# Performance work log

Measured on AMD Instinct MI355X. Metric: run time of the kernel, lower is better.

The kernel has to match this reference:

```python
import jax, jax.numpy as jnp
import numpy as np

B, T, D, H = 32, 2048, 1024, 128


def setup_inputs() -> dict:
    key = jax.random.key(0)
    ks = jax.random.split(key, 7)
    s = 1.0 / np.sqrt(D)
    return {
        "x": jax.random.normal(ks[0], (B, T, D), dtype=jnp.float32),
        "Wk": jax.random.normal(ks[1], (D, H), dtype=jnp.float32) * s,
        "bk": jax.random.normal(ks[2], (H,), dtype=jnp.float32) * 0.01,
        "Wq": jax.random.normal(ks[3], (D, H), dtype=jnp.float32) * s,
        "bq": jax.random.normal(ks[4], (H,), dtype=jnp.float32) * 0.01,
        "Wv": jax.random.normal(ks[5], (D, H), dtype=jnp.float32) * s,
        "bv": jax.random.normal(ks[6], (H,), dtype=jnp.float32) * 0.01,
    }


def reference(x, Wk, bk, Wq, bq, Wv, bv):
    # Single causal attention head. NOTE faithful quirk: scores = K @ Q^T.
    k = x @ Wk + bk  # [B,T,H]
    q = x @ Wq + bq  # [B,T,H]
    v = x @ Wv + bv  # [B,T,H]
    scale = k.shape[-1] ** -0.5
    wei = jnp.einsum("bth,bsh->bts", k, q) * scale  # [B,T,T], K on the left
    t = x.shape[1]
    causal = jnp.tril(jnp.ones((t, t), dtype=bool))
    wei = jnp.where(causal, wei, -jnp.inf)
    wei = jax.nn.softmax(wei, axis=-1)
    # dropout is eval-mode identity (deterministic reference)
    out = jnp.einsum("bts,bsh->bth", wei, v)  # [B,T,H]
    return out
```

## Files before the change

kernel.cpp:

```cpp
#include <hip/hip_runtime.h>
#include <hip/hip_bf16.h>
#include <stdint.h>

typedef __bf16 bf16;
typedef __bf16 bf16x8 __attribute__((ext_vector_type(8)));
typedef __bf16 bf16x4 __attribute__((ext_vector_type(4)));
typedef float f32x4 __attribute__((ext_vector_type(4)));
typedef float f32x8 __attribute__((ext_vector_type(8)));

#define BB 32
#define TT 2048
#define DD 1024
#define HH 128
#define SCALE 0.08838834764831845f
#define LOG2E 1.4426950408889634f
#define KS (SCALE * LOG2E)

__device__ __forceinline__ void gl_lds16(const bf16* g, bf16* l) {
  __builtin_amdgcn_global_load_lds((__attribute__((address_space(1))) const void*)g,
                                   (__attribute__((address_space(3))) void*)l,
                                   16, 0, 0);
}
__device__ __forceinline__ void gl_lds16f_nt(const float* g, float* l) {
  __builtin_amdgcn_global_load_lds((__attribute__((address_space(1))) const void*)g,
                                   (__attribute__((address_space(3))) void*)l,
                                   16, 0, 2);
}

__global__ __launch_bounds__(256) void prep_w(const float* __restrict__ Wk,
                                              const float* __restrict__ Wq,
                                              const float* __restrict__ Wv,
                                              const float* __restrict__ bk,
                                              const float* __restrict__ bq,
                                              const float* __restrict__ bv,
                                              bf16* __restrict__ Wt,
                                              float* __restrict__ bcat) {
  int tid = blockIdx.x * 256 + threadIdx.x;
  if (tid < 384) {
    int mat = tid >> 7, h = tid & 127;
    float bb = (mat == 0) ? bk[h] : (mat == 1) ? bq[h] : bv[h];
    bcat[tid] = (mat == 0) ? bb * KS : bb;
  }
  int mat = tid >> 14;
  int r = tid & 16383;
  int h = r & 127;
  int d0 = (r >> 7) << 3;
  const float* W = (mat == 0) ? Wk : (mat == 1) ? Wq : Wv;
  const float ks = (mat == 0) ? KS : 1.0f;
  bf16x8 v;
#pragma unroll
  for (int i = 0; i < 8; ++i) v[i] = (bf16)(W[(size_t)(d0 + i) * HH + h] * ks);
  *(bf16x8*)(Wt + ((size_t)mat * HH + h) * DD + d0) = v;
}

__global__ __launch_bounds__(256, 2) void qkv_proj(
    const float* __restrict__ x, const bf16* __restrict__ Wt,
    const float* __restrict__ bcat,
    bf16* __restrict__ kb, bf16* __restrict__ qb, bf16* __restrict__ Vt) {
  const int bid = blockIdx.x;
  const int tid = threadIdx.x;
  const int lane = tid & 63;
  const int w = tid >> 6;
  const int l15 = lane & 15, l4 = lane >> 4;
  const size_t row0 = (size_t)bid * 64;
  const int colbase = w * 96;

  __shared__ __attribute__((aligned(16))) float As[2][64][32];
  __shared__ __attribute__((aligned(16))) bf16  Ws[2][384][32];

  f32x4 acc[4][6];
#pragma unroll
  for (int m = 0; m < 4; ++m)
#pragma unroll
    for (int n = 0; n < 6; ++n) acc[m][n] = f32x4{0.f, 0.f, 0.f, 0.f};

  auto stage = [&](int buf, int k0) {
#pragma unroll
    for (int i = 0; i < 2; ++i) {
      int base = i * 256 + w * 64;
      int L = base + lane;
      int r = L >> 3, c = L & 7;
      const float* src = x + (row0 + r) * DD + k0 + ((c ^ (r & 7)) << 2);
      gl_lds16f_nt(src, &As[buf][0][0] + (size_t)base * 4);
    }
#pragma unroll
    for (int i = 0; i < 6; ++i) {
      int base = i * 256 + w * 64;
      int L = base + lane;
      int col = L >> 2, j = L & 3;
      const bf16* src = Wt + (size_t)col * DD + k0 + ((j ^ ((col >> 1) & 3)) << 3);
      gl_lds16(src, &Ws[buf][0][0] + (size_t)base * 8);
    }
  };

  stage(0, 0);
  __syncthreads();

  for (int step = 0; step < 32; ++step) {
    const int cur = step & 1;
    if (step + 1 < 32) stage(cur ^ 1, (step + 1) * 32);

    bf16x8 af[4];
#pragma unroll
    for (int m = 0; m < 4; ++m) {
      int r = m * 16 + l15;
      int c0 = (2 * l4) ^ (r & 7), c1 = (2 * l4 + 1) ^ (r & 7);
      f32x4 lo = *(const f32x4*)&As[cur][r][c0 * 4];
      f32x4 hi = *(const f32x4*)&As[cur][r][c1 * 4];
#pragma unroll
      for (int i = 0; i < 4; ++i) { af[m][i] = (bf16)lo[i]; af[m][4 + i] = (bf16)hi[i]; }
    }
    bf16x8 bfr[6];
#pragma unroll
    for (int n = 0; n < 6; ++n) {
      int col = colbase + n * 16 + l15;
      bfr[n] = *(const bf16x8*)&Ws[cur][col][(l4 ^ ((col >> 1) & 3)) * 8];
    }
#pragma unroll
    for (int m = 0; m < 4; ++m)
#pragma unroll
      for (int n = 0; n < 6; ++n)
        acc[m][n] = __builtin_amdgcn_mfma_f32_16x16x32_bf16(af[m], bfr[n],
                                                            acc[m][n], 0, 0, 0);
    __syncthreads();
  }

  float bvv[6];
#pragma unroll
  for (int n = 0; n < 6; ++n) bvv[n] = bcat[colbase + n * 16 + l15];

  const int bidx = bid >> 5;
  const int tloc0 = (bid & 31) * 64;
#pragma unroll
  for (int m = 0; m < 4; ++m)
#pragma unroll
    for (int n = 0; n < 6; ++n) {
      int col = colbase + n * 16 + l15;
      int mat = col >> 7;
      int hcol = col & 127;
      if (mat == 2) {
        bf16x4 v4;
#pragma unroll
        for (int e = 0; e < 4; ++e) v4[e] = (bf16)(acc[m][n][e] + bvv[n]);
        int t = tloc0 + m * 16 + l4 * 4;
        *(bf16x4*)(Vt + ((size_t)bidx * HH + hcol) * TT + t) = v4;
      } else {
        bf16* dst = (mat == 0) ? kb : qb;
#pragma unroll
        for (int e = 0; e < 4; ++e) {
          size_t rowg = row0 + m * 16 + l4 * 4 + e;
          dst[rowg * HH + hcol] = (bf16)(acc[m][n][e] + bvv[n]);
        }
      }
    }
}

__global__ __launch_bounds__(256, 3) void attn(const bf16* __restrict__ kb,
                                               const bf16* __restrict__ qb,
                                               const bf16* __restrict__ Vt,
                                               float* __restrict__ out) {
  const int bid = blockIdx.x;
  const int b = bid & 31;
  const int p = bid >> 5;
  const int tid = threadIdx.x;
  const int lane = tid & 63;
  const int w = tid >> 6;
  const int l15 = lane & 15, l4 = lane >> 4;

  __shared__ __attribute__((aligned(16))) bf16 Es[64 * 128];
  __shared__ __attribute__((aligned(16))) bf16 Vs[128 * 64];
  __shared__ __attribute__((aligned(16))) bf16 Ps[4][16 * 72];

  for (int job = 0; job < 2; ++job) {
    const int tile = job ? p : (31 - p);
    const int t0 = tile * 64;

    bf16x8 af[4];
    {
      const bf16* kp = kb + ((size_t)b * TT + t0 + w * 16 + l15) * HH + l4 * 8;
#pragma unroll
      for (int kc = 0; kc < 4; ++kc) af[kc] = *(const bf16x8*)(kp + kc * 32);
    }

    f32x4 o[8];
#pragma unroll
    for (int j = 0; j < 8; ++j) o[j] = f32x4{0.f, 0.f, 0.f, 0.f};
    float mrow[4], lrow[4];
#pragma unroll
    for (int e = 0; e < 4; ++e) { mrow[e] = -1e30f; lrow[e] = 0.f; }

    const int nst = tile + 1;
    for (int jt = 0; jt < nst; ++jt) {
      const int s0 = jt * 64;
      {
        const bf16* Eg = qb + ((size_t)b * TT + s0) * HH;
#pragma unroll
        for (int it = 0; it < 4; ++it) {
          int L = w * 256 + it * 64 + lane;
          int er = L >> 4, ec = L & 15;
          int ecs = ec ^ (er & 7);
          gl_lds16(Eg + er * HH + ecs * 8, Es + (size_t)(w * 256 + it * 64) * 8);
        }
        const bf16* Vg = Vt + (size_t)b * HH * TT + s0;
#pragma unroll
        for (int it = 0; it < 4; ++it) {
          int L = w * 256 + it * 64 + lane;
          int vr = L >> 3, vc = L & 7;
          int vcs = vc ^ (vr & 7);
          gl_lds16(Vg + (size_t)vr * TT + vcs * 8, Vs + (size_t)(w * 256 + it * 64) * 8);
        }
      }
      __syncthreads();

      f32x4 s[4];
#pragma unroll
      for (int j = 0; j < 4; ++j) s[j] = f32x4{0.f, 0.f, 0.f, 0.f};
#pragma unroll
      for (int kc = 0; kc < 4; ++kc) {
        bf16x8 ef[4];
#pragma unroll
        for (int fn = 0; fn < 4; ++fn) {
          int er = fn * 16 + l15;
          int c = kc * 4 + l4;
          int cs = c ^ (er & 7);
          ef[fn] = *(const bf16x8*)&Es[er * 128 + cs * 8];
        }
#pragma unroll
        for (int fn = 0; fn < 4; ++fn)
          s[fn] = __builtin_amdgcn_mfma_f32_16x16x32_bf16(af[kc], ef[fn],
                                                          s[fn], 0, 0, 0);
      }

      if (s0 + 63 > t0 + w * 16) {
#pragma unroll
        for (int fn = 0; fn < 4; ++fn)
#pragma unroll
          for (int e = 0; e < 4; ++e) {
            int tg = t0 + w * 16 + l4 * 4 + e;
            int sg = s0 + fn * 16 + l15;
            if (sg > tg) s[fn][e] = -1e30f;
          }
      }

      float mx[4];
#pragma unroll
      for (int e = 0; e < 4; ++e) {
        float m = fmaxf(fmaxf(s[0][e], s[1][e]), fmaxf(s[2][e], s[3][e]));
#pragma unroll
        for (int d = 1; d < 16; d <<= 1) m = fmaxf(m, __shfl_xor(m, d));
        mx[e] = m;
      }
      float g = fmaxf(fmaxf(mx[0] - mrow[0], mx[1] - mrow[1]),
                      fmaxf(mx[2] - mrow[2], mx[3] - mrow[3]));
      if (!__all(g <= 8.0f)) {
#pragma unroll
        for (int e = 0; e < 4; ++e) {
          float mn = fmaxf(mrow[e], mx[e]);
          float rsc = exp2f(mrow[e] - mn);
          lrow[e] *= rsc;
#pragma unroll
          for (int fh = 0; fh < 8; ++fh) o[fh][e] *= rsc;
          mrow[e] = mn;
        }
      }
#pragma unroll
      for (int e = 0; e < 4; ++e) {
        float ps = 0.f;
#pragma unroll
        for (int fn = 0; fn < 4; ++fn) {
          float pv = exp2f(s[fn][e] - mrow[e]);
          s[fn][e] = pv;
          ps += pv;
        }
#pragma unroll
        for (int d = 1; d < 16; d <<= 1) ps += __shfl_xor(ps, d);
        lrow[e] += ps;
      }

#pragma unroll
      for (int fn = 0; fn < 4; ++fn)
#pragma unroll
        for (int e = 0; e < 4; ++e)
          Ps[w][(l4 * 4 + e) * 72 + fn * 16 + l15] = (bf16)s[fn][e];

#pragma unroll
      for (int kc = 0; kc < 2; ++kc) {
        bf16x8 pf = *(const bf16x8*)&Ps[w][l15 * 72 + kc * 32 + l4 * 8];
#pragma unroll
        for (int fh = 0; fh < 8; ++fh) {
          int vr = fh * 16 + l15;
          int c = kc * 4 + l4;
          int cs = c ^ (vr & 7);
          bf16x8 vf = *(const bf16x8*)&Vs[vr * 64 + cs * 8];
          o[fh] = __builtin_amdgcn_mfma_f32_16x16x32_bf16(pf, vf, o[fh], 0, 0, 0);
        }
      }
      __syncthreads();
    }

#pragma unroll
    for (int e = 0; e < 4; ++e) {
      float rl = 1.0f / lrow[e];
      int tg = t0 + w * 16 + l4 * 4 + e;
#pragma unroll
      for (int fh = 0; fh < 8; ++fh)
        out[((size_t)b * TT + tg) * HH + fh * 16 + l15] = o[fh][e] * rl;
    }
  }
}

extern "C" void kernel_launch(void* const* d_in, const int* in_sizes, int n_in,
                              void* d_out, int out_size, void* d_ws, size_t ws_size,
                              hipStream_t stream) {
  (void)in_sizes; (void)n_in; (void)out_size; (void)ws_size;
  const float* x  = (const float*)d_in[0];
  const float* Wk = (const float*)d_in[1];
  const float* bk = (const float*)d_in[2];
  const float* Wq = (const float*)d_in[3];
  const float* bq = (const float*)d_in[4];
  const float* Wv = (const float*)d_in[5];
  const float* bv = (const float*)d_in[6];
  float* out = (float*)d_out;

  const size_t NTH = (size_t)BB * TT * HH;
  bf16* kb = (bf16*)d_ws;
  bf16* qb = kb + NTH;
  bf16* Vt = qb + NTH;
  bf16* Wt = Vt + NTH;
  float* bcat = (float*)(Wt + (size_t)3 * HH * DD);

  prep_w<<<192, 256, 0, stream>>>(Wk, Wq, Wv, bk, bq, bv, Wt, bcat);
  qkv_proj<<<1024, 256, 0, stream>>>(x, Wt, bcat, kb, qb, Vt);
  attn<<<512, 256, 0, stream>>>(kb, qb, Vt, out);
}
```

Before: 211.4 us.

## Enlarge QKV projection tile to 256 rows with 8 waves and bf16 x staging

The QKV projection now uses 512-thread blocks, each computing 256 rows by 384 columns, so every block of W staged into LDS is reused across four times as many rows. The x tile is loaded into registers, converted to bf16 once and written to a padded bf16 LDS buffer, replacing the direct fp32 global-to-LDS load and the per-wave conversions. This reduces repeated W loads and LDS footprint per row. In exchange the grid drops to 256 blocks (about one per CU), there are twice as many accumulators per wave, which raises register pressure, and x loads go through registers, which may expose their latency.

```diff
diff --git a/kernel.cpp b/kernel.cpp
--- a/kernel.cpp
+++ b/kernel.cpp
@@ -20,11 +20,6 @@
   __builtin_amdgcn_global_load_lds((__attribute__((address_space(1))) const void*)g,
                                    (__attribute__((address_space(3))) void*)l,
                                    16, 0, 0);
-}
-__device__ __forceinline__ void gl_lds16f_nt(const float* g, float* l) {
-  __builtin_amdgcn_global_load_lds((__attribute__((address_space(1))) const void*)g,
-                                   (__attribute__((address_space(3))) void*)l,
-                                   16, 0, 2);
 }
 
 __global__ __launch_bounds__(256) void prep_w(const float* __restrict__ Wk,
@@ -53,7 +48,7 @@
   *(bf16x8*)(Wt + ((size_t)mat * HH + h) * DD + d0) = v;
 }
 
-__global__ __launch_bounds__(256, 2) void qkv_proj(
+__global__ __launch_bounds__(512, 2) void qkv_proj(
     const float* __restrict__ x, const bf16* __restrict__ Wt,
     const float* __restrict__ bcat,
     bf16* __restrict__ kb, bf16* __restrict__ qb, bf16* __restrict__ Vt) {
@@ -61,67 +56,79 @@
   const int tid = threadIdx.x;
   const int lane = tid & 63;
   const int w = tid >> 6;
+  const int wr = w >> 2, wc = w & 3;
   const int l15 = lane & 15, l4 = lane >> 4;
-  const size_t row0 = (size_t)bid * 64;
-  const int colbase = w * 96;
-
-  __shared__ __attribute__((aligned(16))) float As[2][64][32];
-  __shared__ __attribute__((aligned(16))) bf16  Ws[2][384][32];
-
-  f32x4 acc[4][6];
-#pragma unroll
-  for (int m = 0; m < 4; ++m)
+  const size_t row0 = (size_t)bid * 256;
+  const int colbase = wc * 96;
+  const int rowbase = wr * 128;
+
+  __shared__ __attribute__((aligned(16))) bf16 As[2][256][40];
+  __shared__ __attribute__((aligned(16))) bf16 Ws[2][384 * 32];
+
+  const int sxr = tid >> 1, sxh = (tid & 1) * 16;
+
+  f32x4 acc[8][6];
+#pragma unroll
+  for (int m = 0; m < 8; ++m)
 #pragma unroll
     for (int n = 0; n < 6; ++n) acc[m][n] = f32x4{0.f, 0.f, 0.f, 0.f};
 
-  auto stage = [&](int buf, int k0) {
-#pragma unroll
-    for (int i = 0; i < 2; ++i) {
-      int base = i * 256 + w * 64;
-      int L = base + lane;
-      int r = L >> 3, c = L & 7;
-      const float* src = x + (row0 + r) * DD + k0 + ((c ^ (r & 7)) << 2);
-      gl_lds16f_nt(src, &As[buf][0][0] + (size_t)base * 4);
-    }
-#pragma unroll
-    for (int i = 0; i < 6; ++i) {
-      int base = i * 256 + w * 64;
+  auto stage_w = [&](int buf, int k0) {
+#pragma unroll
+    for (int i = 0; i < 3; ++i) {
+      int base = i * 512 + (w << 6);
       int L = base + lane;
       int col = L >> 2, j = L & 3;
       const bf16* src = Wt + (size_t)col * DD + k0 + ((j ^ ((col >> 1) & 3)) << 3);
-      gl_lds16(src, &Ws[buf][0][0] + (size_t)base * 8);
+      gl_lds16(src, &Ws[buf][0] + (size_t)base * 8);
     }
   };
-
-  stage(0, 0);
+  auto write_x = [&](int buf, f32x8 a0, f32x8 a1) {
+    bf16x8 t0, t1;
+#pragma unroll
+    for (int i = 0; i < 8; ++i) { t0[i] = (bf16)a0[i]; t1[i] = (bf16)a1[i]; }
+    *(bf16x8*)&As[buf][sxr][sxh] = t0;
+    *(bf16x8*)&As[buf][sxr][sxh + 8] = t1;
+  };
+
+  {
+    const float* src = x + (row0 + sxr) * DD + sxh;
+    f32x8 a0 = *(const f32x8*)src;
+    f32x8 a1 = *(const f32x8*)(src + 8);
+    stage_w(0, 0);
+    write_x(0, a0, a1);
+  }
   __syncthreads();
 
   for (int step = 0; step < 32; ++step) {
     const int cur = step & 1;
-    if (step + 1 < 32) stage(cur ^ 1, (step + 1) * 32);
-
-    bf16x8 af[4];
-#pragma unroll
-    for (int m = 0; m < 4; ++m) {
-      int r = m * 16 + l15;
-      int c0 = (2 * l4) ^ (r & 7), c1 = (2 * l4 + 1) ^ (r & 7);
-      f32x4 lo = *(const f32x4*)&As[cur][r][c0 * 4];
-      f32x4 hi = *(const f32x4*)&As[cur][r][c1 * 4];
-#pragma unroll
-      for (int i = 0; i < 4; ++i) { af[m][i] = (bf16)lo[i]; af[m][4 + i] = (bf16)hi[i]; }
-    }
+    const int k0 = step * 32;
+
+    f32x8 a0, a1;
+    if (step < 31) {
+      const float* src = x + (row0 + sxr) * DD + k0 + 32 + sxh;
+      a0 = *(const f32x8*)src;
+      a1 = *(const f32x8*)(src + 8);
+      stage_w(cur ^ 1, k0 + 32);
+    }
+
     bf16x8 bfr[6];
 #pragma unroll
     for (int n = 0; n < 6; ++n) {
       int col = colbase + n * 16 + l15;
-      bfr[n] = *(const bf16x8*)&Ws[cur][col][(l4 ^ ((col >> 1) & 3)) * 8];
-    }
-#pragma unroll
-    for (int m = 0; m < 4; ++m)
+      bfr[n] = *(const bf16x8*)&Ws[cur][col * 32 + ((l4 ^ ((col >> 1) & 3)) << 3)];
+    }
+#pragma unroll
+    for (int m = 0; m < 8; ++m) {
+      int r = rowbase + m * 16 + l15;
+      bf16x8 afm = *(const bf16x8*)&As[cur][r][l4 * 8];
 #pragma unroll
       for (int n = 0; n < 6; ++n)
-        acc[m][n] = __builtin_amdgcn_mfma_f32_16x16x32_bf16(af[m], bfr[n],
+        acc[m][n] = __builtin_amdgcn_mfma_f32_16x16x32_bf16(afm, bfr[n],
                                                             acc[m][n], 0, 0, 0);
+    }
+
+    if (step < 31) write_x(cur ^ 1, a0, a1);
     __syncthreads();
   }
 
@@ -129,28 +136,26 @@
 #pragma unroll
   for (int n = 0; n < 6; ++n) bvv[n] = bcat[colbase + n * 16 + l15];
 
-  const int bidx = bid >> 5;
-  const int tloc0 = (bid & 31) * 64;
-#pragma unroll
-  for (int m = 0; m < 4; ++m)
+  const int bidx = bid >> 3;
+  const int tloc0 = (bid & 7) * 256;
+#pragma unroll
+  for (int m = 0; m < 8; ++m)
 #pragma unroll
     for (int n = 0; n < 6; ++n) {
       int col = colbase + n * 16 + l15;
       int mat = col >> 7;
       int hcol = col & 127;
+      int rloc = rowbase + m * 16 + l4 * 4;
       if (mat == 2) {
         bf16x4 v4;
 #pragma unroll
         for (int e = 0; e < 4; ++e) v4[e] = (bf16)(acc[m][n][e] + bvv[n]);
-        int t = tloc0 + m * 16 + l4 * 4;
-        *(bf16x4*)(Vt + ((size_t)bidx * HH + hcol) * TT + t) = v4;
+        *(bf16x4*)(Vt + ((size_t)bidx * HH + hcol) * TT + tloc0 + rloc) = v4;
       } else {
         bf16* dst = (mat == 0) ? kb : qb;
 #pragma unroll
-        for (int e = 0; e < 4; ++e) {
-          size_t rowg = row0 + m * 16 + l4 * 4 + e;
-          dst[rowg * HH + hcol] = (bf16)(acc[m][n][e] + bvv[n]);
-        }
+        for (int e = 0; e < 4; ++e)
+          dst[(row0 + rloc + e) * HH + hcol] = (bf16)(acc[m][n][e] + bvv[n]);
       }
     }
 }
@@ -330,6 +335,6 @@
   float* bcat = (float*)(Wt + (size_t)3 * HH * DD);
 
   prep_w<<<192, 256, 0, stream>>>(Wk, Wq, Wv, bk, bq, bv, Wt, bcat);
-  qkv_proj<<<1024, 256, 0, stream>>>(x, Wt, bcat, kb, qb, Vt);
+  qkv_proj<<<256, 512, 0, stream>>>(x, Wt, bcat, kb, qb, Vt);
   attn<<<512, 256, 0, stream>>>(kb, qb, Vt, out);
 }
```

Measured after the change: 191.7 us. 1.1x faster.
